# Kernel tuning notes

Measured on AMD Instinct MI355X. Metric: run time of the kernel, lower is better.

The kernel has to match this reference:

```python
import jax, jax.numpy as jnp
import numpy as np

NEG_INF = -9e15


def setup_inputs() -> dict:
    key = jax.random.key(0)
    k1, k2, k3, k4, k5 = jax.random.split(key, 5)
    N, F_IN, F_OUT = 8192, 512, 256
    x = jax.random.normal(k1, (N, F_IN), dtype=jnp.float32)
    adjacent_matrix = jax.random.randint(k2, (N, N), 0, 2, dtype=jnp.int32)
    # xavier-normal-like scales (gain sqrt(2))
    W = jax.random.normal(k3, (F_IN, F_OUT), dtype=jnp.float32) * np.sqrt(2.0) * np.sqrt(2.0 / (F_IN + F_OUT))
    a1 = jax.random.normal(k4, (F_OUT, 1), dtype=jnp.float32) * np.sqrt(2.0) * np.sqrt(2.0 / (F_OUT + 1))
    a2 = jax.random.normal(k5, (F_OUT, 1), dtype=jnp.float32) * np.sqrt(2.0) * np.sqrt(2.0 / (F_OUT + 1))
    return {"x": x, "adjacent_matrix": adjacent_matrix, "W": W, "a1": a1, "a2": a2}


def reference(x, adjacent_matrix, W, a1, a2):
    alpha = 0.2  # LeakyReLU negative slope
    h = x @ W                                   # [N, F_out]
    f1 = h @ a1                                 # [N, 1]
    f2 = h @ a2                                 # [N, 1]
    e = f1 + f2.T                               # [N, N] broadcast pairwise scores
    e = jnp.where(e > 0, e, alpha * e)          # LeakyReLU
    e = jnp.where(adjacent_matrix > 0, e, NEG_INF)  # mask non-edges
    attention = jax.nn.softmax(e, axis=1)       # [N, N]
    h_prime = attention @ h                     # [N, F_out]
    return jax.nn.elu(h_prime)                  # concat=True -> ELU
```

## Files before the change

kernel.cpp:

```cpp
#include <hip/hip_runtime.h>
#include <hip/hip_bf16.h>

#define N_NODES 8192
#define F_IN 512
#define F_OUT 256
#define KSPLIT 8
#define KCHUNK (N_NODES / KSPLIT)
#define NTILES (KCHUNK / 32)
#define ROWSB 128

using short8 = __attribute__((ext_vector_type(8))) short;
using f32x4  = __attribute__((ext_vector_type(4))) float;

typedef __attribute__((address_space(3))) void lds_t;
typedef const __attribute__((address_space(1))) void gbl_t;

__device__ __forceinline__ short f2bf(float v) {
    union { float f; unsigned u; } x; x.f = v;
    unsigned r = x.u + 0x7fffu + ((x.u >> 16) & 1u);
    return (short)(r >> 16);
}

__global__ void k_prep(const float* __restrict__ W, const float* __restrict__ a1,
                       const float* __restrict__ a2, float* __restrict__ w1,
                       float* __restrict__ w2, short* __restrict__ WTg) {
    const int k = blockIdx.x;
    const int l = threadIdx.x;
    float4 wv = *(const float4*)(W + (size_t)k * F_OUT + 4 * l);
    float4 av = *(const float4*)(a1 + 4 * l);
    float4 bv = *(const float4*)(a2 + 4 * l);
    float s1 = wv.x*av.x + wv.y*av.y + wv.z*av.z + wv.w*av.w;
    float s2 = wv.x*bv.x + wv.y*bv.y + wv.z*bv.z + wv.w*bv.w;
    WTg[(size_t)(4*l+0)*F_IN + k] = f2bf(wv.x);
    WTg[(size_t)(4*l+1)*F_IN + k] = f2bf(wv.y);
    WTg[(size_t)(4*l+2)*F_IN + k] = f2bf(wv.z);
    WTg[(size_t)(4*l+3)*F_IN + k] = f2bf(wv.w);
    #pragma unroll
    for (int off = 32; off; off >>= 1) {
        s1 += __shfl_down(s1, off);
        s2 += __shfl_down(s2, off);
    }
    if (l == 0) { w1[k] = s1; w2[k] = s2; }
}

__global__ void k_f12(const float* __restrict__ x, const float* __restrict__ w1,
                      const float* __restrict__ w2, float* __restrict__ f1,
                      float* __restrict__ f2) {
    const int wv = threadIdx.x >> 6, l = threadIdx.x & 63;
    const int i = blockIdx.x * 4 + wv;
    const float* xr = x + (size_t)i * F_IN;
    float s1 = 0.f, s2 = 0.f;
    #pragma unroll
    for (int t = 0; t < 2; ++t) {
        int k = t * 256 + l * 4;
        float4 xv = *(const float4*)(xr + k);
        float4 u  = *(const float4*)(w1 + k);
        float4 v  = *(const float4*)(w2 + k);
        s1 += xv.x*u.x + xv.y*u.y + xv.z*u.z + xv.w*u.w;
        s2 += xv.x*v.x + xv.y*v.y + xv.z*v.z + xv.w*v.w;
    }
    #pragma unroll
    for (int off = 32; off; off >>= 1) {
        s1 += __shfl_down(s1, off);
        s2 += __shfl_down(s2, off);
    }
    if (l == 0) { f1[i] = s1; f2[i] = s2; }
}

__launch_bounds__(256)
__global__ void k_hT(const float* __restrict__ x, const short* __restrict__ WTg,
                     short* __restrict__ hT) {
    __shared__ short x_lds[32 * 64];
    __shared__ short wt_lds[256 * 64];
    const int tid = threadIdx.x;
    const int wv = tid >> 6, l = tid & 63, lg = l >> 4, lr = l & 15;
    const int ibase = blockIdx.x * 32;
    f32x4 acc[4][2];
    #pragma unroll
    for (int a = 0; a < 4; ++a)
        #pragma unroll
        for (int b = 0; b < 2; ++b) acc[a][b] = (f32x4){0.f, 0.f, 0.f, 0.f};
    for (int k0 = 0; k0 < F_IN; k0 += 64) {
        __syncthreads();
        {
            int i = tid >> 3, ch = tid & 7;
            const float* src = x + (size_t)(ibase + i) * F_IN + k0 + ch * 8;
            float4 v0 = *(const float4*)(src);
            float4 v1 = *(const float4*)(src + 4);
            short8 s;
            s[0]=f2bf(v0.x); s[1]=f2bf(v0.y); s[2]=f2bf(v0.z); s[3]=f2bf(v0.w);
            s[4]=f2bf(v1.x); s[5]=f2bf(v1.y); s[6]=f2bf(v1.z); s[7]=f2bf(v1.w);
            *(short8*)&x_lds[i * 64 + 8 * (ch ^ (i & 7))] = s;
        }
        {
            int cb = tid >> 3, ch = tid & 7;
            #pragma unroll
            for (int p = 0; p < 8; ++p) {
                int c = cb + 32 * p;
                short8 s = *(const short8*)(WTg + (size_t)c * F_IN + k0 + ch * 8);
                *(short8*)&wt_lds[c * 64 + 8 * (ch ^ (c & 7))] = s;
            }
        }
        __syncthreads();
        #pragma unroll
        for (int ks = 0; ks < 2; ++ks) {
            short8 bfrag[2], afrag[4];
            #pragma unroll
            for (int it = 0; it < 2; ++it) {
                int i = it * 16 + lr;
                bfrag[it] = *(short8*)&x_lds[i * 64 + 8 * ((lg + 4*ks) ^ (i & 7))];
            }
            #pragma unroll
            for (int ct = 0; ct < 4; ++ct) {
                int c = wv * 64 + ct * 16 + lr;
                afrag[ct] = *(short8*)&wt_lds[c * 64 + 8 * ((lg + 4*ks) ^ (c & 7))];
            }
            #pragma unroll
            for (int ct = 0; ct < 4; ++ct)
                #pragma unroll
                for (int it = 0; it < 2; ++it)
                    acc[ct][it] = __builtin_amdgcn_mfma_f32_16x16x32_bf16(
                        afrag[ct], bfrag[it], acc[ct][it], 0, 0, 0);
        }
    }
    #pragma unroll
    for (int ct = 0; ct < 4; ++ct)
        #pragma unroll
        for (int it = 0; it < 2; ++it)
            #pragma unroll
            for (int r = 0; r < 4; ++r) {
                int c = wv * 64 + ct * 16 + 4 * lg + r;
                int i = ibase + it * 16 + lr;
                hT[(size_t)c * N_NODES + i] = f2bf(acc[ct][it][r]);
            }
}

__launch_bounds__(256, 2)
__global__ void k_attn(const int* __restrict__ adj, const short* __restrict__ hT,
                       const float* __restrict__ f1, const float* __restrict__ f2,
                       float* __restrict__ part, float* __restrict__ psum) {
    __shared__ short h_lds[4 * 8192];
    __shared__ float f2_lds[KCHUNK];
    const int tid = threadIdx.x;
    const int wv = tid >> 6, l = tid & 63, lg = l >> 4, lr = l & 15;
    const int ksid = blockIdx.x & 7;
    const int rowblk = blockIdx.x >> 3;
    const int r0 = rowblk * ROWSB;
    const int row0 = r0 + wv * 32 + lr;
    const int row1 = row0 + 16;
    const int kbeg = ksid * KCHUNK;
    const short* hsrcb = hT + (size_t)(wv * 16 + (l >> 2)) * N_NODES + kbeg
                            + ((l & 3) ^ ((l >> 2) & 3)) * 8;
    const int* asrcb = adj + (size_t)(r0 + wv * 32 + (l >> 1)) * N_NODES + kbeg + (l & 1) * 16;
    const float f1v0 = f1[row0];
    const float f1v1 = f1[row1];
    const float L2E = 1.44269504f;
    f32x4 acc0[16], acc1[16];
    #pragma unroll
    for (int t = 0; t < 16; ++t) {
        acc0[t] = (f32x4){0.f, 0.f, 0.f, 0.f};
        acc1[t] = (f32x4){0.f, 0.f, 0.f, 0.f};
    }
    float ps0 = 0.f, ps1 = 0.f;

    int4 SA[4], SB[4];
    unsigned mA, mB;

#define STAGE(T) do {                                                           \
    _Pragma("unroll")                                                           \
    for (int p = 0; p < 4; ++p)                                                 \
        __builtin_amdgcn_global_load_lds(                                       \
            (gbl_t*)(hsrcb + (size_t)p * 64 * N_NODES + (T) * 32),              \
            (lds_t*)&h_lds[((T) & 3) * 8192 + p * 2048 + wv * 512], 16, 0, 0);  \
} while (0)

#define ADJ(S, T) do {                                                          \
    S[0] = *(const int4*)(asrcb + (T) * 32);                                    \
    S[1] = *(const int4*)(asrcb + (T) * 32 + 4);                                \
    S[2] = *(const int4*)(asrcb + (T) * 32 + 8);                                \
    S[3] = *(const int4*)(asrcb + (T) * 32 + 12);                               \
} while (0)

#define PACK(MD, S) do {                                                        \
    unsigned _m = 0;                                                            \
    _Pragma("unroll")                                                           \
    for (int qq = 0; qq < 4; ++qq) {                                            \
        _m |= (S[qq].x > 0 ? 1u : 0u) << (qq * 4);                              \
        _m |= (S[qq].y > 0 ? 2u : 0u) << (qq * 4);                              \
        _m |= (S[qq].z > 0 ? 4u : 0u) << (qq * 4);                              \
        _m |= (S[qq].w > 0 ? 8u : 0u) << (qq * 4);                              \
    }                                                                           \
    unsigned _a0 = (unsigned)__shfl((int)_m, (lr << 1) | (lg >> 1));            \
    unsigned _a1 = (unsigned)__shfl((int)_m, ((16 + lr) << 1) | (lg >> 1));     \
    MD = ((_a0 >> (8 * (lg & 1))) & 0xffu) |                                    \
         (((_a1 >> (8 * (lg & 1))) & 0xffu) << 8);                              \
} while (0)

#define COMPUTE(T, MD) do {                                                     \
    const int bo = ((T) & 3) * 8192;                                            \
    const float4 fa = *(const float4*)&f2_lds[(T) * 32 + lg * 8];               \
    const float4 fb4 = *(const float4*)&f2_lds[(T) * 32 + lg * 8 + 4];          \
    const float f2v[8] = {fa.x, fa.y, fa.z, fa.w, fb4.x, fb4.y, fb4.z, fb4.w};  \
    short8 pa0, pa1;                                                            \
    _Pragma("unroll")                                                           \
    for (int j = 0; j < 8; ++j) {                                               \
        float e0 = f1v0 + f2v[j];                                               \
        float e1 = f1v1 + f2v[j];                                               \
        float le0 = fmaxf(e0, 0.2f * e0);                                       \
        float le1 = fmaxf(e1, 0.2f * e1);                                       \
        float p0 = ((MD) & (1u << j)) ? exp2f(fminf(le0 * L2E, 80.f)) : 0.f;    \
        float p1 = ((MD) & (256u << j)) ? exp2f(fminf(le1 * L2E, 80.f)) : 0.f;  \
        ps0 += p0; ps1 += p1;                                                   \
        pa0[j] = f2bf(p0); pa1[j] = f2bf(p1);                                   \
    }                                                                           \
    __builtin_amdgcn_s_setprio(1);                                              \
    _Pragma("unroll")                                                           \
    for (int t16 = 0; t16 < 16; ++t16) {                                        \
        short8 bfrag = *(short8*)&h_lds[bo + t16 * 512 + lr * 32                \
                                        + (lg ^ (lr & 3)) * 8];                 \
        acc0[t16] = __builtin_amdgcn_mfma_f32_16x16x32_bf16(pa0, bfrag, acc0[t16], 0, 0, 0); \
        acc1[t16] = __builtin_amdgcn_mfma_f32_16x16x32_bf16(pa1, bfrag, acc1[t16], 0, 0, 0); \
    }                                                                           \
    __builtin_amdgcn_s_setprio(0);                                              \
} while (0)

#define BODY(T, SCUR, MCUR, SNXT, MNXT) do {                                    \
    PACK(MNXT, SNXT);                                    \
    ADJ(SCUR, (T) + 2);                                                         \
    STAGE((T) + 2);                                                             \
    asm volatile("s_waitcnt vmcnt(12)" ::: "memory");                           \
    __builtin_amdgcn_s_barrier();                                               \
    __builtin_amdgcn_sched_barrier(0);                                          \
    COMPUTE(T, MCUR);                                                           \
} while (0)

    ADJ(SA, 0); ADJ(SB, 1);
    STAGE(0); STAGE(1);
    *(float4*)&f2_lds[tid * 4] = *(const float4*)(f2 + kbeg + tid * 4);
    PACK(mA, SA);
    __syncthreads();

    for (int t = 0; t < NTILES - 2; t += 2) {
        BODY(t,     SA, mA, SB, mB);
        BODY(t + 1, SB, mB, SA, mA);
    }
    {
        PACK(mB, SB);
        __builtin_amdgcn_s_barrier();
        __builtin_amdgcn_sched_barrier(0);
        COMPUTE(NTILES - 2, mA);
    }
    {
        asm volatile("s_waitcnt vmcnt(0)" ::: "memory");
        __builtin_amdgcn_s_barrier();
        __builtin_amdgcn_sched_barrier(0);
        COMPUTE(NTILES - 1, mB);
    }
#undef STAGE
#undef ADJ
#undef PACK
#undef COMPUTE
#undef BODY

    ps0 += __shfl_xor(ps0, 16);
    ps0 += __shfl_xor(ps0, 32);
    ps1 += __shfl_xor(ps1, 16);
    ps1 += __shfl_xor(ps1, 32);
    if (lg == 0) {
        psum[ksid * N_NODES + row0] = ps0;
        psum[ksid * N_NODES + row1] = ps1;
    }
    float* pb = part + (size_t)ksid * N_NODES * F_OUT;
    #pragma unroll
    for (int t = 0; t < 16; ++t)
        #pragma unroll
        for (int r = 0; r < 4; ++r) {
            int c = t * 16 + lr;
            int rr0 = r0 + wv * 32 + 4 * lg + r;
            pb[(size_t)rr0 * F_OUT + c] = acc0[t][r];
            pb[(size_t)(rr0 + 16) * F_OUT + c] = acc1[t][r];
        }
}

__global__ void k_comb(const float* __restrict__ part, const float* __restrict__ psum,
                       float* __restrict__ out) {
    const int i = blockIdx.x, c = threadIdx.x;
    float o = 0.f, s = 0.f;
    #pragma unroll
    for (int qq = 0; qq < KSPLIT; ++qq) {
        o += part[(size_t)qq * N_NODES * F_OUT + (size_t)i * F_OUT + c];
        s += psum[qq * N_NODES + i];
    }
    float v = o / s;
    out[(size_t)i * F_OUT + c] = (v > 0.f) ? v : expm1f(v);
}

extern "C" void kernel_launch(void* const* d_in, const int* in_sizes, int n_in,
                              void* d_out, int out_size, void* d_ws, size_t ws_size,
                              hipStream_t stream) {
    const float* x  = (const float*)d_in[0];
    const int* adj  = (const int*)d_in[1];
    const float* W  = (const float*)d_in[2];
    const float* a1 = (const float*)d_in[3];
    const float* a2 = (const float*)d_in[4];
    float* out = (float*)d_out;

    short* hT  = (short*)d_ws;
    short* WTg = hT + (size_t)F_OUT * N_NODES;
    float* fb  = (float*)(WTg + (size_t)F_OUT * F_IN);
    float* w1   = fb;
    float* w2   = fb + 512;
    float* f1   = fb + 1024;
    float* f2   = fb + 1024 + N_NODES;
    float* part = fb + 32768;
    float* psum = part + (size_t)KSPLIT * N_NODES * F_OUT;

    k_prep<<<F_IN, 64, 0, stream>>>(W, a1, a2, w1, w2, WTg);
    k_f12<<<N_NODES / 4, 256, 0, stream>>>(x, w1, w2, f1, f2);
    k_hT<<<N_NODES / 32, 256, 0, stream>>>(x, WTg, hT);
    k_attn<<<(N_NODES / ROWSB) * KSPLIT, 256, 0, stream>>>(adj, hT, f1, f2, part, psum);
    k_comb<<<N_NODES, 256, 0, stream>>>(part, psum, out);
}
```

Baseline: 480.9 us.

## Load h fragments directly from global memory instead of staging through LDS

Measured after the change: 690.5 us. +43.6%, slower.

```diff
diff --git a/kernel.cpp b/kernel.cpp
--- a/kernel.cpp
+++ b/kernel.cpp
@@ -11,9 +11,6 @@
 
 using short8 = __attribute__((ext_vector_type(8))) short;
 using f32x4  = __attribute__((ext_vector_type(4))) float;
-
-typedef __attribute__((address_space(3))) void lds_t;
-typedef const __attribute__((address_space(1))) void gbl_t;
 
 __device__ __forceinline__ short f2bf(float v) {
     union { float f; unsigned u; } x; x.f = v;
@@ -139,8 +136,6 @@
 __global__ void k_attn(const int* __restrict__ adj, const short* __restrict__ hT,
                        const float* __restrict__ f1, const float* __restrict__ f2,
                        float* __restrict__ part, float* __restrict__ psum) {
-    __shared__ short h_lds[4 * 8192];
-    __shared__ float f2_lds[KCHUNK];
     const int tid = threadIdx.x;
     const int wv = tid >> 6, l = tid & 63, lg = l >> 4, lr = l & 15;
     const int ksid = blockIdx.x & 7;
@@ -149,8 +144,7 @@
     const int row0 = r0 + wv * 32 + lr;
     const int row1 = row0 + 16;
     const int kbeg = ksid * KCHUNK;
-    const short* hsrcb = hT + (size_t)(wv * 16 + (l >> 2)) * N_NODES + kbeg
-                            + ((l & 3) ^ ((l >> 2) & 3)) * 8;
+    const short* hfl = hT + (size_t)lr * N_NODES + kbeg + lg * 8;
     const int* asrcb = adj + (size_t)(r0 + wv * 32 + (l >> 1)) * N_NODES + kbeg + (l & 1) * 16;
     const float f1v0 = f1[row0];
     const float f1v1 = f1[row1];
@@ -163,16 +157,8 @@
     }
     float ps0 = 0.f, ps1 = 0.f;
 
-    int4 SA[4], SB[4];
+    int4 S0[4], S1[4], S2[4], S3[4];
     unsigned mA, mB;
-
-#define STAGE(T) do {                                                           \
-    _Pragma("unroll")                                                           \
-    for (int p = 0; p < 4; ++p)                                                 \
-        __builtin_amdgcn_global_load_lds(                                       \
-            (gbl_t*)(hsrcb + (size_t)p * 64 * N_NODES + (T) * 32),              \
-            (lds_t*)&h_lds[((T) & 3) * 8192 + p * 2048 + wv * 512], 16, 0, 0);  \
-} while (0)
 
 #define ADJ(S, T) do {                                                          \
     S[0] = *(const int4*)(asrcb + (T) * 32);                                    \
@@ -197,9 +183,12 @@
 } while (0)
 
 #define COMPUTE(T, MD) do {                                                     \
-    const int bo = ((T) & 3) * 8192;                                            \
-    const float4 fa = *(const float4*)&f2_lds[(T) * 32 + lg * 8];               \
-    const float4 fb4 = *(const float4*)&f2_lds[(T) * 32 + lg * 8 + 4];          \
+    short8 bf[8];                                                               \
+    _Pragma("unroll")                                                           \
+    for (int t16 = 0; t16 < 8; ++t16)                                           \
+        bf[t16] = *(const short8*)(hfl + (size_t)(t16 * 16) * N_NODES + (T) * 32); \
+    const float4 fa = *(const float4*)(f2 + kbeg + (T) * 32 + lg * 8);          \
+    const float4 fb4 = *(const float4*)(f2 + kbeg + (T) * 32 + lg * 8 + 4);     \
     const float f2v[8] = {fa.x, fa.y, fa.z, fa.w, fb4.x, fb4.y, fb4.z, fb4.w};  \
     short8 pa0, pa1;                                                            \
     _Pragma("unroll")                                                           \
@@ -215,48 +204,38 @@
     }                                                                           \
     __builtin_amdgcn_s_setprio(1);                                              \
     _Pragma("unroll")                                                           \
-    for (int t16 = 0; t16 < 16; ++t16) {                                        \
-        short8 bfrag = *(short8*)&h_lds[bo + t16 * 512 + lr * 32                \
-                                        + (lg ^ (lr & 3)) * 8];                 \
-        acc0[t16] = __builtin_amdgcn_mfma_f32_16x16x32_bf16(pa0, bfrag, acc0[t16], 0, 0, 0); \
-        acc1[t16] = __builtin_amdgcn_mfma_f32_16x16x32_bf16(pa1, bfrag, acc1[t16], 0, 0, 0); \
+    for (int t16 = 0; t16 < 8; ++t16) {                                         \
+        acc0[t16] = __builtin_amdgcn_mfma_f32_16x16x32_bf16(pa0, bf[t16], acc0[t16], 0, 0, 0); \
+        acc1[t16] = __builtin_amdgcn_mfma_f32_16x16x32_bf16(pa1, bf[t16], acc1[t16], 0, 0, 0); \
+    }                                                                           \
+    __builtin_amdgcn_s_setprio(0);                                              \
+    _Pragma("unroll")                                                           \
+    for (int t16 = 0; t16 < 8; ++t16)                                           \
+        bf[t16] = *(const short8*)(hfl + (size_t)((t16 + 8) * 16) * N_NODES + (T) * 32); \
+    __builtin_amdgcn_s_setprio(1);                                              \
+    _Pragma("unroll")                                                           \
+    for (int t16 = 0; t16 < 8; ++t16) {                                         \
+        acc0[t16 + 8] = __builtin_amdgcn_mfma_f32_16x16x32_bf16(pa0, bf[t16], acc0[t16 + 8], 0, 0, 0); \
+        acc1[t16 + 8] = __builtin_amdgcn_mfma_f32_16x16x32_bf16(pa1, bf[t16], acc1[t16 + 8], 0, 0, 0); \
     }                                                                           \
     __builtin_amdgcn_s_setprio(0);                                              \
 } while (0)
 
-#define BODY(T, SCUR, MCUR, SNXT, MNXT) do {                                    \
-    PACK(MNXT, SNXT);                                    \
-    ADJ(SCUR, (T) + 2);                                                         \
-    STAGE((T) + 2);                                                             \
-    asm volatile("s_waitcnt vmcnt(12)" ::: "memory");                           \
-    __builtin_amdgcn_s_barrier();                                               \
-    __builtin_amdgcn_sched_barrier(0);                                          \
+#define BODY(T, SNXT, SREF, MCUR, MNXT) do {                                    \
+    PACK(MNXT, SNXT);                                                           \
+    if ((T) + 4 < NTILES) ADJ(SREF, (T) + 4);                                   \
     COMPUTE(T, MCUR);                                                           \
 } while (0)
 
-    ADJ(SA, 0); ADJ(SB, 1);
-    STAGE(0); STAGE(1);
-    *(float4*)&f2_lds[tid * 4] = *(const float4*)(f2 + kbeg + tid * 4);
-    PACK(mA, SA);
-    __syncthreads();
-
-    for (int t = 0; t < NTILES - 2; t += 2) {
-        BODY(t,     SA, mA, SB, mB);
-        BODY(t + 1, SB, mB, SA, mA);
-    }
-    {
-        PACK(mB, SB);
-        __builtin_amdgcn_s_barrier();
-        __builtin_amdgcn_sched_barrier(0);
-        COMPUTE(NTILES - 2, mA);
-    }
-    {
-        asm volatile("s_waitcnt vmcnt(0)" ::: "memory");
-        __builtin_amdgcn_s_barrier();
-        __builtin_amdgcn_sched_barrier(0);
-        COMPUTE(NTILES - 1, mB);
-    }
-#undef STAGE
+    ADJ(S0, 0); ADJ(S1, 1); ADJ(S2, 2); ADJ(S3, 3);
+    PACK(mA, S0);
+
+    for (int t = 0; t < NTILES; t += 4) {
+        BODY(t,     S1, S0, mA, mB);
+        BODY(t + 1, S2, S1, mB, mA);
+        BODY(t + 2, S3, S2, mA, mB);
+        BODY(t + 3, S0, S3, mB, mA);
+    }
 #undef ADJ
 #undef PACK
 #undef COMPUTE
```
